# Kernel tuning notes

Hardware: AMD Instinct MI355X
Metric: run time of the kernel (lower is better)

## Reference

```python
import jax, jax.numpy as jnp
import numpy as np

B, I, H = 65536, 256, 256

def setup_inputs() -> dict:
    key = jax.random.key(0)
    ks = jax.random.split(key, 7)
    stdv = 1.0 / np.sqrt(H)
    u = lambda k, shape: jax.random.uniform(k, shape, jnp.float32, -stdv, stdv)
    return {
        "x":  jax.random.normal(ks[0], (B, I), jnp.float32),
        "h":  jax.random.normal(ks[1], (B, H), jnp.float32),
        "c":  jax.random.normal(ks[2], (B, H), jnp.float32),
        "Wi": u(ks[3], (4, H, I)),   # stacked [W_ii, W_if, W_ig, W_io], torch layout [out,in]
        "Wh": u(ks[4], (4, H, H)),   # stacked [W_hi, W_hf, W_hg, W_ho]
        "bi": u(ks[5], (4, H)),
        "bh": u(ks[6], (4, H)),
    }

def reference(x, h, c, Wi, Wh, bi, bh):
    # Fused version of 8 separate Linears: two batched GEMMs + one elementwise pass.
    # gates[b, k, h] = x @ Wi[k].T + h_prev @ Wh[k].T + bi[k] + bh[k]
    gates = (jnp.einsum('bi,khi->bkh', x, Wi)
             + jnp.einsum('bj,khj->bkh', h, Wh)
             + bi[None] + bh[None])
    i = jax.nn.sigmoid(gates[:, 0])
    f = jax.nn.sigmoid(gates[:, 1])
    g = jnp.tanh(gates[:, 2])
    o = jax.nn.sigmoid(gates[:, 3])
    c_new = f * c + i * g
    h_new = o * jnp.tanh(c_new)
    return (h_new, c_new)
```

## Files before the change

kernel.cpp:

```cpp
#include <hip/hip_runtime.h>
#include <stdint.h>

#define B_DIM 65536
#define HOFF  16777216

typedef __attribute__((ext_vector_type(8))) short short8;
typedef __attribute__((ext_vector_type(8))) unsigned short ushort8_t;
typedef __attribute__((ext_vector_type(4))) float f32x4;

__device__ __forceinline__ unsigned short f2bf(float f) {
  unsigned int u = __builtin_bit_cast(unsigned int, f);
  u += 0x7FFFu + ((u >> 16) & 1u);
  return (unsigned short)(u >> 16);
}
__device__ __forceinline__ float sigf(float x) { return 1.0f / (1.0f + __expf(-x)); }
__device__ __forceinline__ float tanh_fast(float x) {
  float a = fabsf(x);
  float e = __expf(-2.0f * a);
  float t = (1.0f - e) / (1.0f + e);
  return x < 0.0f ? -t : t;
}

typedef const __attribute__((address_space(1))) unsigned int* as1p;
typedef __attribute__((address_space(3))) unsigned int* as3p;
__device__ __forceinline__ void llds16(const unsigned short* g, unsigned short* l) {
  __builtin_amdgcn_global_load_lds((as1p)g, (as3p)l, 16, 0, 0);
}

__global__ void prep_a(const float* __restrict__ x, const float* __restrict__ h,
                       ushort8_t* __restrict__ A8) {
  unsigned o = blockIdx.x * 256u + threadIdx.x;
  unsigned b = o >> 6, c8 = o & 63u;
  const float* src = (c8 < 32u) ? x + (size_t)b * 256u + c8 * 8u
                                : h + (size_t)b * 256u + (c8 - 32u) * 8u;
  float4 v0 = *(const float4*)src;
  float4 v1 = *(const float4*)(src + 4);
  ushort8_t p;
  p[0] = f2bf(v0.x); p[1] = f2bf(v0.y); p[2] = f2bf(v0.z); p[3] = f2bf(v0.w);
  p[4] = f2bf(v1.x); p[5] = f2bf(v1.y); p[6] = f2bf(v1.z); p[7] = f2bf(v1.w);
  A8[o] = p;
}

__global__ void prep_w(const float* __restrict__ Wi, const float* __restrict__ Wh,
                       ushort8_t* __restrict__ W8) {
  unsigned o = blockIdx.x * 256u + threadIdx.x;
  unsigned n = o >> 6, c8 = o & 63u;
  const float* src = (c8 < 32u) ? Wi + (size_t)n * 256u + c8 * 8u
                                : Wh + (size_t)n * 256u + (c8 - 32u) * 8u;
  float4 v0 = *(const float4*)src;
  float4 v1 = *(const float4*)(src + 4);
  ushort8_t p;
  p[0] = f2bf(v0.x); p[1] = f2bf(v0.y); p[2] = f2bf(v0.z); p[3] = f2bf(v0.w);
  p[4] = f2bf(v1.x); p[5] = f2bf(v1.y); p[6] = f2bf(v1.z); p[7] = f2bf(v1.w);
  W8[o] = p;
}

__global__ __launch_bounds__(256, 3) void lstm_gemm(
    const unsigned short* __restrict__ A,
    const unsigned short* __restrict__ W,
    const float* __restrict__ cprev,
    const float* __restrict__ bi, const float* __restrict__ bh,
    float* __restrict__ out) {
  __shared__ __align__(16) char smem[32768];
  unsigned short* sA = (unsigned short*)smem;
  unsigned short* sB = (unsigned short*)(smem + 16384);

  const int t = threadIdx.x;
  const int wid = t >> 6, lane = t & 63;
  const int m = lane & 15, q = lane >> 4;

  const unsigned bid = blockIdx.x;
  const unsigned xcd = bid & 7u, kk_ = bid >> 3;
  const int b0 = (int)((xcd * 64u + (kk_ >> 3)) * 128u);
  const int h0 = (int)((kk_ & 7u) * 32u);

  const int R = (wid >> 1) * 64, Cc = (wid & 1) * 64;
  const int hcol = h0 + ((Cc >> 6) << 4) + m;

  const int l4 = lane >> 2;
  const int sg0 = wid * 2, sg1 = wid * 2 + 1;
  const int r0 = sg0 * 16 + l4, r1 = sg1 * 16 + l4;
  const int ck = ((lane & 3) ^ ((l4 >> 1) & 3)) * 8;
  const unsigned aO0 = (unsigned)(b0 + r0) * 512u + (unsigned)ck;
  const unsigned aO1 = (unsigned)(b0 + r1) * 512u + (unsigned)ck;
  const int n0 = (((r0 >> 4) & 3) << 8) + h0 + (r0 & 15) + ((r0 >> 6) << 4);
  const int n1 = (((r1 >> 4) & 3) << 8) + h0 + (r1 & 15) + ((r1 >> 6) << 4);
  const unsigned wO0 = (unsigned)n0 * 512u + (unsigned)ck;
  const unsigned wO1 = (unsigned)n1 * 512u + (unsigned)ck;
  unsigned short* dA0 = sA + sg0 * 512;
  unsigned short* dA1 = sA + sg1 * 512;
  unsigned short* dB0 = sB + sg0 * 512;
  unsigned short* dB1 = sB + sg1 * 512;

  const int swz = (q ^ ((m >> 1) & 3)) * 8;

  f32x4 acc[4][4];
#pragma unroll
  for (int j = 0; j < 4; ++j) {
    float bv = bi[(j << 8) + hcol] + bh[(j << 8) + hcol];
    f32x4 z = {bv, bv, bv, bv};
#pragma unroll
    for (int i = 0; i < 4; ++i) acc[i][j] = z;
  }

  for (int kt = 0; kt < 8; ++kt) {
    const unsigned k0 = kt * 64u;
    llds16(A + aO0 + k0, dA0);
    llds16(A + aO1 + k0, dA1);
    llds16(W + wO0 + k0, dB0);
    llds16(W + wO1 + k0, dB1);
    llds16(A + aO0 + k0 + 32u, dA0 + 4096);
    llds16(A + aO1 + k0 + 32u, dA1 + 4096);
    llds16(W + wO0 + k0 + 32u, dB0 + 4096);
    llds16(W + wO1 + k0 + 32u, dB1 + 4096);
    __syncthreads();
    {
      short8 av[4], bv[4];
#pragma unroll
      for (int i = 0; i < 4; ++i)
        av[i] = *(const short8*)&sA[(R + i * 16 + m) * 32 + swz];
#pragma unroll
      for (int j = 0; j < 4; ++j)
        bv[j] = *(const short8*)&sB[(Cc + j * 16 + m) * 32 + swz];
#pragma unroll
      for (int i = 0; i < 4; ++i)
#pragma unroll
        for (int j = 0; j < 4; ++j)
          acc[i][j] = __builtin_amdgcn_mfma_f32_16x16x32_bf16(av[i], bv[j], acc[i][j], 0, 0, 0);
    }
    {
      short8 av[4], bv[4];
#pragma unroll
      for (int i = 0; i < 4; ++i)
        av[i] = *(const short8*)&sA[4096 + (R + i * 16 + m) * 32 + swz];
#pragma unroll
      for (int j = 0; j < 4; ++j)
        bv[j] = *(const short8*)&sB[4096 + (Cc + j * 16 + m) * 32 + swz];
#pragma unroll
      for (int i = 0; i < 4; ++i)
#pragma unroll
        for (int j = 0; j < 4; ++j)
          acc[i][j] = __builtin_amdgcn_mfma_f32_16x16x32_bf16(av[i], bv[j], acc[i][j], 0, 0, 0);
    }
    __syncthreads();
  }

  const float* cp = cprev + hcol;
  float hn[4][4], cn[4][4];
#pragma unroll
  for (int i = 0; i < 4; ++i) {
    const int br = b0 + R + i * 16 + (q << 2);
    float cv[4];
#pragma unroll
    for (int r = 0; r < 4; ++r) cv[r] = cp[(size_t)(br + r) << 8];
#pragma unroll
    for (int r = 0; r < 4; ++r) {
      float iv = sigf(acc[i][0][r]);
      float fv = sigf(acc[i][1][r]);
      float gv = tanh_fast(acc[i][2][r]);
      float ov = sigf(acc[i][3][r]);
      float c2 = fv * cv[r] + iv * gv;
      cn[i][r] = c2;
      hn[i][r] = ov * tanh_fast(c2);
    }
  }

  float* ep = (float*)smem;
  const int ecol = ((Cc >> 6) << 4) + m;
#pragma unroll
  for (int i = 0; i < 4; ++i)
#pragma unroll
    for (int r = 0; r < 4; ++r)
      ep[(R + i * 16 + (q << 2) + r) * 36 + ecol] = hn[i][r];
  __syncthreads();
#pragma unroll
  for (int k = 0; k < 4; ++k) {
    const int id = t + k * 256;
    const int row = id >> 3, c4 = id & 7;
    *(float4*)(out + ((size_t)(b0 + row) << 8) + h0 + c4 * 4) =
        *(const float4*)&ep[row * 36 + c4 * 4];
  }
  __syncthreads();
#pragma unroll
  for (int i = 0; i < 4; ++i)
#pragma unroll
    for (int r = 0; r < 4; ++r)
      ep[(R + i * 16 + (q << 2) + r) * 36 + ecol] = cn[i][r];
  __syncthreads();
#pragma unroll
  for (int k = 0; k < 4; ++k) {
    const int id = t + k * 256;
    const int row = id >> 3, c4 = id & 7;
    *(float4*)(out + HOFF + ((size_t)(b0 + row) << 8) + h0 + c4 * 4) =
        *(const float4*)&ep[row * 36 + c4 * 4];
  }
}

__global__ void lstm_naive(const float* __restrict__ x, const float* __restrict__ h,
                           const float* __restrict__ c,
                           const float* __restrict__ Wi, const float* __restrict__ Wh,
                           const float* __restrict__ bi, const float* __restrict__ bh,
                           float* __restrict__ out) {
  int gid = blockIdx.x * 256 + threadIdx.x;
  int b = gid >> 8, hh = gid & 255;
  float a0 = bi[hh] + bh[hh];
  float a1 = bi[256 + hh] + bh[256 + hh];
  float a2 = bi[512 + hh] + bh[512 + hh];
  float a3 = bi[768 + hh] + bh[768 + hh];
  const float* xr = x + (size_t)b * 256;
  const float* hr = h + (size_t)b * 256;
  const float* w0 = Wi + (size_t)hh * 256;
  const float* w1 = Wh + (size_t)hh * 256;
  for (int i = 0; i < 256; ++i) {
    float xv = xr[i];
    a0 += xv * w0[i]; a1 += xv * w0[65536 + i];
    a2 += xv * w0[131072 + i]; a3 += xv * w0[196608 + i];
  }
  for (int i = 0; i < 256; ++i) {
    float hv = hr[i];
    a0 += hv * w1[i]; a1 += hv * w1[65536 + i];
    a2 += hv * w1[131072 + i]; a3 += hv * w1[196608 + i];
  }
  float iv = sigf(a0), fv = sigf(a1), gv = tanh_fast(a2), ov = sigf(a3);
  float cn = fv * c[gid] + iv * gv;
  out[gid] = ov * tanh_fast(cn);
  out[HOFF + gid] = cn;
}

extern "C" void kernel_launch(void* const* d_in, const int* in_sizes, int n_in,
                              void* d_out, int out_size, void* d_ws, size_t ws_size,
                              hipStream_t stream) {
  const float* x  = (const float*)d_in[0];
  const float* h  = (const float*)d_in[1];
  const float* c  = (const float*)d_in[2];
  const float* Wi = (const float*)d_in[3];
  const float* Wh = (const float*)d_in[4];
  const float* bi = (const float*)d_in[5];
  const float* bh = (const float*)d_in[6];
  float* out = (float*)d_out;

  const size_t needA = (size_t)B_DIM * 512 * 2;
  const size_t needW = (size_t)1024 * 512 * 2;
  if (ws_size >= needA + needW) {
    ushort8_t* A8 = (ushort8_t*)d_ws;
    ushort8_t* W8 = (ushort8_t*)((char*)d_ws + needA);
    hipLaunchKernelGGL(prep_a, dim3(B_DIM * 64 / 256), dim3(256), 0, stream, x, h, A8);
    hipLaunchKernelGGL(prep_w, dim3(1024 * 64 / 256), dim3(256), 0, stream, Wi, Wh, W8);
    hipLaunchKernelGGL(lstm_gemm, dim3((B_DIM / 128) * 8), dim3(256), 0, stream,
                       (const unsigned short*)A8, (const unsigned short*)W8,
                       c, bi, bh, out);
  } else {
    hipLaunchKernelGGL(lstm_naive, dim3(B_DIM), dim3(256), 0, stream,
                       x, h, c, Wi, Wh, bi, bh, out);
  }
}
```

Measured before the change: 360.3 us.

## Double-buffer LDS tiles, prefetch cell state, and merge epilogue stores

Switches the GEMM K-loop to two LDS buffers so the next tile's global-to-LDS loads are issued before the MFMAs on the current tile run, which drops one barrier per iteration. The previous cell state is loaded during the last K iteration, hiding its latency behind compute. The epilogue stages h and c in separate LDS regions so a single barrier covers both, instead of two staging passes. In exchange, LDS per block doubles to 64KB and launch bounds drop from 3 to 2 blocks per CU, which lowers occupancy. The kernel also has to rely on the async LDS load completing before the one remaining barrier.

```diff
diff --git a/kernel.cpp b/kernel.cpp
--- a/kernel.cpp
+++ b/kernel.cpp
@@ -55,15 +55,14 @@
   W8[o] = p;
 }
 
-__global__ __launch_bounds__(256, 3) void lstm_gemm(
+__global__ __launch_bounds__(256, 2) void lstm_gemm(
     const unsigned short* __restrict__ A,
     const unsigned short* __restrict__ W,
     const float* __restrict__ cprev,
     const float* __restrict__ bi, const float* __restrict__ bh,
     float* __restrict__ out) {
-  __shared__ __align__(16) char smem[32768];
-  unsigned short* sA = (unsigned short*)smem;
-  unsigned short* sB = (unsigned short*)(smem + 16384);
+  __shared__ __align__(16) char smem[65536];
+  unsigned short* const base = (unsigned short*)smem;
 
   const int t = threadIdx.x;
   const int wid = t >> 6, lane = t & 63;
@@ -87,10 +86,7 @@
   const int n1 = (((r1 >> 4) & 3) << 8) + h0 + (r1 & 15) + ((r1 >> 6) << 4);
   const unsigned wO0 = (unsigned)n0 * 512u + (unsigned)ck;
   const unsigned wO1 = (unsigned)n1 * 512u + (unsigned)ck;
-  unsigned short* dA0 = sA + sg0 * 512;
-  unsigned short* dA1 = sA + sg1 * 512;
-  unsigned short* dB0 = sB + sg0 * 512;
-  unsigned short* dB1 = sB + sg1 * 512;
+  const int dst0 = sg0 * 512, dst1 = sg1 * 512;
 
   const int swz = (q ^ ((m >> 1) & 3)) * 8;
 
@@ -103,25 +99,48 @@
     for (int i = 0; i < 4; ++i) acc[i][j] = z;
   }
 
+  auto stage = [&](int buf, unsigned k0) {
+    unsigned short* sAb = base + buf * 16384;
+    unsigned short* sBb = sAb + 8192;
+    llds16(A + aO0 + k0, sAb + dst0);
+    llds16(A + aO1 + k0, sAb + dst1);
+    llds16(W + wO0 + k0, sBb + dst0);
+    llds16(W + wO1 + k0, sBb + dst1);
+    llds16(A + aO0 + k0 + 32u, sAb + dst0 + 4096);
+    llds16(A + aO1 + k0 + 32u, sAb + dst1 + 4096);
+    llds16(W + wO0 + k0 + 32u, sBb + dst0 + 4096);
+    llds16(W + wO1 + k0 + 32u, sBb + dst1 + 4096);
+  };
+
+  const float* cp = cprev + hcol;
+  float cv[4][4];
+
+  stage(0, 0u);
+  __syncthreads();
+
+#pragma unroll
   for (int kt = 0; kt < 8; ++kt) {
-    const unsigned k0 = kt * 64u;
-    llds16(A + aO0 + k0, dA0);
-    llds16(A + aO1 + k0, dA1);
-    llds16(W + wO0 + k0, dB0);
-    llds16(W + wO1 + k0, dB1);
-    llds16(A + aO0 + k0 + 32u, dA0 + 4096);
-    llds16(A + aO1 + k0 + 32u, dA1 + 4096);
-    llds16(W + wO0 + k0 + 32u, dB0 + 4096);
-    llds16(W + wO1 + k0 + 32u, dB1 + 4096);
-    __syncthreads();
+    const int cur = kt & 1;
+    if (kt < 7) {
+      stage(cur ^ 1, (unsigned)(kt + 1) * 64u);
+    } else {
+#pragma unroll
+      for (int i = 0; i < 4; ++i) {
+        const int br = b0 + R + i * 16 + (q << 2);
+#pragma unroll
+        for (int r = 0; r < 4; ++r) cv[i][r] = cp[(size_t)(br + r) << 8];
+      }
+    }
+    const unsigned short* sAb = base + cur * 16384;
+    const unsigned short* sBb = sAb + 8192;
     {
       short8 av[4], bv[4];
 #pragma unroll
       for (int i = 0; i < 4; ++i)
-        av[i] = *(const short8*)&sA[(R + i * 16 + m) * 32 + swz];
+        av[i] = *(const short8*)&sAb[(R + i * 16 + m) * 32 + swz];
 #pragma unroll
       for (int j = 0; j < 4; ++j)
-        bv[j] = *(const short8*)&sB[(Cc + j * 16 + m) * 32 + swz];
+        bv[j] = *(const short8*)&sBb[(Cc + j * 16 + m) * 32 + swz];
 #pragma unroll
       for (int i = 0; i < 4; ++i)
 #pragma unroll
@@ -132,10 +151,10 @@
       short8 av[4], bv[4];
 #pragma unroll
       for (int i = 0; i < 4; ++i)
-        av[i] = *(const short8*)&sA[4096 + (R + i * 16 + m) * 32 + swz];
+        av[i] = *(const short8*)&sAb[4096 + (R + i * 16 + m) * 32 + swz];
 #pragma unroll
       for (int j = 0; j < 4; ++j)
-        bv[j] = *(const short8*)&sB[4096 + (Cc + j * 16 + m) * 32 + swz];
+        bv[j] = *(const short8*)&sBb[4096 + (Cc + j * 16 + m) * 32 + swz];
 #pragma unroll
       for (int i = 0; i < 4; ++i)
 #pragma unroll
@@ -145,54 +164,41 @@
     __syncthreads();
   }
 
-  const float* cp = cprev + hcol;
   float hn[4][4], cn[4][4];
 #pragma unroll
   for (int i = 0; i < 4; ++i) {
-    const int br = b0 + R + i * 16 + (q << 2);
-    float cv[4];
-#pragma unroll
-    for (int r = 0; r < 4; ++r) cv[r] = cp[(size_t)(br + r) << 8];
 #pragma unroll
     for (int r = 0; r < 4; ++r) {
       float iv = sigf(acc[i][0][r]);
       float fv = sigf(acc[i][1][r]);
       float gv = tanh_fast(acc[i][2][r]);
       float ov = sigf(acc[i][3][r]);
-      float c2 = fv * cv[r] + iv * gv;
+      float c2 = fv * cv[i][r] + iv * gv;
       cn[i][r] = c2;
       hn[i][r] = ov * tanh_fast(c2);
     }
   }
 
-  float* ep = (float*)smem;
+  float* eph = (float*)smem;
+  float* epc = eph + 4608;
   const int ecol = ((Cc >> 6) << 4) + m;
 #pragma unroll
   for (int i = 0; i < 4; ++i)
 #pragma unroll
-    for (int r = 0; r < 4; ++r)
-      ep[(R + i * 16 + (q << 2) + r) * 36 + ecol] = hn[i][r];
+    for (int r = 0; r < 4; ++r) {
+      const int row = R + i * 16 + (q << 2) + r;
+      eph[row * 36 + ecol] = hn[i][r];
+      epc[row * 36 + ecol] = cn[i][r];
+    }
   __syncthreads();
 #pragma unroll
   for (int k = 0; k < 4; ++k) {
     const int id = t + k * 256;
     const int row = id >> 3, c4 = id & 7;
     *(float4*)(out + ((size_t)(b0 + row) << 8) + h0 + c4 * 4) =
-        *(const float4*)&ep[row * 36 + c4 * 4];
-  }
-  __syncthreads();
-#pragma unroll
-  for (int i = 0; i < 4; ++i)
-#pragma unroll
-    for (int r = 0; r < 4; ++r)
-      ep[(R + i * 16 + (q << 2) + r) * 36 + ecol] = cn[i][r];
-  __syncthreads();
-#pragma unroll
-  for (int k = 0; k < 4; ++k) {
-    const int id = t + k * 256;
-    const int row = id >> 3, c4 = id & 7;
+        *(const float4*)&eph[row * 36 + c4 * 4];
     *(float4*)(out + HOFF + ((size_t)(b0 + row) << 8) + h0 + c4 * 4) =
-        *(const float4*)&ep[row * 36 + c4 * 4];
+        *(const float4*)&epc[row * 36 + c4 * 4];
   }
 }
 
```

Result: slower. 374.3 us (+3.9%).
